# Kernel tuning notes

Measured on AMD Instinct MI355X. Metric: run time of the kernel, lower is better.

Reference implementation:

```python
import jax, jax.numpy as jnp
import numpy as np

B, S, H, NH = 2, 2048, 1024, 16
HD = H // NH  # head_size = 64


def setup_inputs() -> dict:
    key = jax.random.key(0)
    ks = jax.random.split(key, 9)
    sc = 0.02
    return {
        "hidden_states": jax.random.normal(ks[0], (B, S, H), dtype=jnp.float32),
        "Wq": jax.random.normal(ks[1], (H, H), dtype=jnp.float32) * sc,
        "bq": jax.random.normal(ks[2], (H,), dtype=jnp.float32) * sc,
        "Wk": jax.random.normal(ks[3], (H, H), dtype=jnp.float32) * sc,
        "bk": jax.random.normal(ks[4], (H,), dtype=jnp.float32) * sc,
        "Wv": jax.random.normal(ks[5], (H, H), dtype=jnp.float32) * sc,
        "bv": jax.random.normal(ks[6], (H,), dtype=jnp.float32) * sc,
        "Wo": jax.random.normal(ks[7], (H, H), dtype=jnp.float32) * sc,
        "bo": jax.random.normal(ks[8], (H,), dtype=jnp.float32) * sc,
    }


def reference(hidden_states, Wq, bq, Wk, bk, Wv, bv, Wo, bo):
    b, s, h = hidden_states.shape
    # nn.Linear: y = x @ W.T + b
    q = hidden_states @ Wq.T + bq
    k = hidden_states @ Wk.T + bk
    v = hidden_states @ Wv.T + bv
    q = q.reshape(b, s, NH, HD)
    k = k.reshape(b, s, NH, HD)
    v = v.reshape(b, s, NH, HD)
    # scores: [b, heads, q, k]
    scores = jnp.einsum("bqhd,bkhd->bhqk", q, k) / jnp.sqrt(jnp.float32(HD))
    # causal mask: triu(ones, diagonal=1) positions set to -inf
    causal = jnp.triu(jnp.ones((s, s), dtype=bool), k=1)
    scores = jnp.where(causal[None, None], -jnp.inf, scores)
    attn = jax.nn.softmax(scores, axis=-1)
    ctx = jnp.einsum("bhqk,bkhd->bqhd", attn, v).reshape(b, s, h)
    return ctx @ Wo.T + bo
```

## Files before the change

kernel.cpp:

```cpp
#include <hip/hip_runtime.h>
#include <hip/hip_bf16.h>

#define B_  2
#define S_  2048
#define H_  1024
#define NH_ 16
#define HD_ 64

typedef unsigned short u16;
typedef unsigned int   u32;
typedef __attribute__((ext_vector_type(4))) float  f32x4;
typedef __attribute__((ext_vector_type(8))) __bf16 bf16x8;
typedef __attribute__((ext_vector_type(2))) unsigned int u32x2;
typedef __attribute__((ext_vector_type(4))) unsigned short u16x4;

__device__ __forceinline__ u16 f2bf(float f) {
  unsigned u = __builtin_bit_cast(unsigned, f);
  u += 0x7fffu + ((u >> 16) & 1u);
  return (u16)(u >> 16);
}
__device__ __forceinline__ u32 cvtpk(float lo, float hi) {
  u32 r;
  asm("v_cvt_pk_bf16_f32 %0, %1, %2" : "=v"(r) : "v"(lo), "v"(hi));
  return r;
}
__device__ __forceinline__ float ex2(float x) {
  float r;
  asm("v_exp_f32 %0, %1" : "=v"(r) : "v"(x));
  return r;
}

__device__ __forceinline__ void gload_lds16(const void* g, void* l) {
  __builtin_amdgcn_global_load_lds(
      (const __attribute__((address_space(1))) void*)g,
      (__attribute__((address_space(3))) void*)l, 16, 0, 0);
}

#define NX_ (4u * 1024u * 1024u)
__global__ __launch_bounds__(256) void cvt_all(const float* __restrict__ x,
                                               const float* __restrict__ w0, const float* __restrict__ w1,
                                               const float* __restrict__ w2, const float* __restrict__ w3,
                                               u16* __restrict__ xb,
                                               u16* __restrict__ o0, u16* __restrict__ o1,
                                               u16* __restrict__ o2, u16* __restrict__ o3) {
  size_t i4 = ((size_t)blockIdx.x * 256 + threadIdx.x) * 4;
  const float* src; u16* dst; size_t off;
  if (i4 < (size_t)NX_) { src = x; dst = xb; off = i4; }
  else {
    size_t j = i4 - NX_;
    int seg = (int)(j >> 20);
    off = j & ((1u << 20) - 1);
    src = seg == 0 ? w0 : seg == 1 ? w1 : seg == 2 ? w2 : w3;
    dst = seg == 0 ? o0 : seg == 1 ? o1 : seg == 2 ? o2 : o3;
  }
  float4 v = *reinterpret_cast<const float4*>(src + off);
  u16x4 o;
  o[0] = f2bf(v.x); o[1] = f2bf(v.y); o[2] = f2bf(v.z); o[3] = f2bf(v.w);
  *reinterpret_cast<u16x4*>(dst + off) = o;
}

__device__ __forceinline__ void store_out(float* C, size_t idx, float v) { C[idx] = v; }
__device__ __forceinline__ void store_out(u16* C, size_t idx, float v) { C[idx] = f2bf(v); }

template <int MI, typename OutT>
__device__ __forceinline__ void gemm_core(const u16* __restrict__ A, const u16* __restrict__ Bw,
                                          const float* __restrict__ bias, OutT* __restrict__ C,
                                          int M, int N, int K, float oscale, int m0, int n0,
                                          u16* lsA, u16* lsB) {
  const int t = threadIdx.x;
  const int w = t >> 6, lane = t & 63;
  const int g = lane >> 4, c = lane & 15;
  const int wr = w >> 1, wc = w & 1;

  f32x4 acc[MI][4] = {};
  const int rowS = w * 16 + (lane >> 2);
  const int colS = (lane & 3) * 8;

  for (int k0 = 0; k0 < K; k0 += 32) {
    __syncthreads();
#pragma unroll
    for (int r = 0; r < MI / 2; ++r)
      gload_lds16(A + (size_t)(m0 + r * 64 + rowS) * K + k0 + colS, lsA + r * 2048 + w * 512);
#pragma unroll
    for (int r = 0; r < 2; ++r)
      gload_lds16(Bw + (size_t)(n0 + r * 64 + rowS) * K + k0 + colS, lsB + r * 2048 + w * 512);
    asm volatile("s_waitcnt vmcnt(0)" ::: "memory");
    __syncthreads();

    bf16x8 af[MI], bfr[4];
#pragma unroll
    for (int mi = 0; mi < MI; ++mi)
      af[mi] = *reinterpret_cast<const bf16x8*>(&lsA[(wr * (MI * 16) + mi * 16 + c) * 32 + g * 8]);
#pragma unroll
    for (int ni = 0; ni < 4; ++ni)
      bfr[ni] = *reinterpret_cast<const bf16x8*>(&lsB[(wc * 64 + ni * 16 + c) * 32 + g * 8]);
#pragma unroll
    for (int mi = 0; mi < MI; ++mi)
#pragma unroll
      for (int ni = 0; ni < 4; ++ni)
        acc[mi][ni] = __builtin_amdgcn_mfma_f32_16x16x32_bf16(af[mi], bfr[ni], acc[mi][ni], 0, 0, 0);
  }

#pragma unroll
  for (int mi = 0; mi < MI; ++mi) {
    int rowb = m0 + wr * (MI * 16) + mi * 16 + g * 4;
#pragma unroll
    for (int ni = 0; ni < 4; ++ni) {
      int col = n0 + wc * 64 + ni * 16 + c;
      float bv = bias[col];
#pragma unroll
      for (int r = 0; r < 4; ++r) {
        float v = (acc[mi][ni][r] + bv) * oscale;
        store_out(C, (size_t)(rowb + r) * N + col, v);
      }
    }
  }
}

__global__ __launch_bounds__(256) void gemm_qkv(const u16* __restrict__ xb,
                                                const u16* __restrict__ Wq, const u16* __restrict__ Wk,
                                                const u16* __restrict__ Wv,
                                                const float* __restrict__ bq, const float* __restrict__ bk,
                                                const float* __restrict__ bv,
                                                u16* __restrict__ Q, u16* __restrict__ Kb, u16* __restrict__ Vb,
                                                int M, int K, float qscale) {
  __shared__ u16 lsA[4096];
  __shared__ u16 lsB[4096];
  const int fid = blockIdx.x;
  const int xcd = fid & 7, i = fid >> 3;
  const int mloc = i / 24, nn = i % 24;
  const int m0 = (xcd * 4 + mloc) * 128;
  const int ng = nn * 128;
  const int sel = ng >> 10, n0 = ng & 1023;
  const u16*  W    = sel == 0 ? Wq : sel == 1 ? Wk : Wv;
  const float* bia = sel == 0 ? bq : sel == 1 ? bk : bv;
  u16*        Cp   = sel == 0 ? Q  : sel == 1 ? Kb : Vb;
  float os = sel == 0 ? qscale : 1.0f;
  gemm_core<4, u16>(xb, W, bia, Cp, M, 1024, K, os, m0, n0, lsA, lsB);
}

__global__ __launch_bounds__(256) void gemm_wo(const u16* __restrict__ A, const u16* __restrict__ Bw,
                                               const float* __restrict__ bias, float* __restrict__ C,
                                               int M, int N, int K) {
  __shared__ u16 lsA[2048];
  __shared__ u16 lsB[4096];
  const int fid = blockIdx.x;
  const int xcd = fid & 7, i = fid >> 3;
  const int mloc = i >> 3, nn = i & 7;
  const int m0 = (xcd * 8 + mloc) * 64;
  const int n0 = nn * 128;
  gemm_core<2, float>(A, Bw, bias, C, M, N, K, 1.0f, m0, n0, lsA, lsB);
}

__device__ __forceinline__ void stage_k(const u16* __restrict__ Kg, size_t headoff, int kvb,
                                        int kRow0, int kColB, int w, u16* lsKbuf) {
#pragma unroll
  for (int r = 0; r < 2; ++r)
    gload_lds16((const char*)(Kg + headoff + (size_t)(kvb + r * 32 + kRow0) * H_) + kColB,
                (char*)lsKbuf + r * 4096 + w * 1024);
}

__global__ __launch_bounds__(256) void attn_fwd(const u16* __restrict__ Qg,
                                                const u16* __restrict__ Kg,
                                                const u16* __restrict__ Vg,
                                                u16* __restrict__ Og) {
  __shared__ u16 lsK[2][64 * 64];
  __shared__ u16 lsVt[2][64 * 72];
  __shared__ u16 lsP[4][16 * 72];

  const int blk = blockIdx.x;
  const int xcd = blk & 7, i = blk >> 3;
  const int pair = i & 3;
  const int qt = 31 - (i >> 2);
  const int bh = xcd * 4 + pair;
  const int h = bh & 15, b = bh >> 4;

  const int t = threadIdx.x, w = t >> 6, lane = t & 63;
  const int g = lane >> 4, c = lane & 15;
  const size_t headoff = (size_t)b * (S_ * H_) + (size_t)h * HD_;
  const int q0 = qt * 64 + w * 16;
  const int nt = qt + 1;

  const int kO    = w * 1024 + lane * 16;
  const int kRow0 = kO >> 7;
  const int kColB = (kO & 127) ^ ((kRow0 & 7) << 4);
  const int vKv = 2 * (t >> 4);
  const int vD0 = 4 * (t & 15);
  const int vS  = 8 * ((vD0 >> 3) & 7);

  int qkOff[4][2], pvOff[4][2];
#pragma unroll
  for (int nj = 0; nj < 4; ++nj) {
    int krow = nj * 16 + c, sw = (krow & 7) << 4;
    qkOff[nj][0] = krow * 128 + ((g * 16) ^ sw);
    qkOff[nj][1] = krow * 128 + ((64 + g * 16) ^ sw);
  }
#pragma unroll
  for (int dt = 0; dt < 4; ++dt) {
    int d = dt * 16 + c, sx = ((d >> 3) & 7) << 4;
    pvOff[dt][0] = d * 144 + ((g * 16) ^ sx);
    pvOff[dt][1] = d * 144 + ((64 + g * 16) ^ sx);
  }

  bf16x8 aq0 = *reinterpret_cast<const bf16x8*>(Qg + headoff + (size_t)(q0 + c) * H_ + g * 8);
  bf16x8 aq1 = *reinterpret_cast<const bf16x8*>(Qg + headoff + (size_t)(q0 + c) * H_ + 32 + g * 8);

  f32x4 oacc[4] = {};
  float mrun = -1e30f, lrun = 0.f;
  u32x2 vlo[2], vhi[2];

#pragma unroll
  for (int r = 0; r < 2; ++r) {
    const u16* vp = Vg + headoff + (size_t)(r * 32 + vKv) * H_ + vD0;
    vlo[r] = *reinterpret_cast<const u32x2*>(vp);
    vhi[r] = *reinterpret_cast<const u32x2*>(vp + H_);
  }
  stage_k(Kg, headoff, 0, kRow0, kColB, w, lsK[0]);
  asm volatile("s_waitcnt vmcnt(2)" ::: "memory");
#pragma unroll
  for (int r = 0; r < 2; ++r) {
    int kvx = (r * 32 + vKv) ^ vS;
    u32 w0 = __builtin_amdgcn_perm(vhi[r][0], vlo[r][0], 0x05040100u);
    u32 w1 = __builtin_amdgcn_perm(vhi[r][0], vlo[r][0], 0x07060302u);
    u32 w2 = __builtin_amdgcn_perm(vhi[r][1], vlo[r][1], 0x05040100u);
    u32 w3 = __builtin_amdgcn_perm(vhi[r][1], vlo[r][1], 0x07060302u);
    *reinterpret_cast<u32*>(&lsVt[0][(vD0 + 0) * 72 + kvx]) = w0;
    *reinterpret_cast<u32*>(&lsVt[0][(vD0 + 1) * 72 + kvx]) = w1;
    *reinterpret_cast<u32*>(&lsVt[0][(vD0 + 2) * 72 + kvx]) = w2;
    *reinterpret_cast<u32*>(&lsVt[0][(vD0 + 3) * 72 + kvx]) = w3;
  }
  __syncthreads();

  for (int kt = 0; kt < nt; ++kt) {
    const int cur = kt & 1;
    const int kv0 = kt * 64;
    const bool st = (kt + 1 < nt);
    if (st) {
#pragma unroll
      for (int r = 0; r < 2; ++r) {
        const u16* vp = Vg + headoff + (size_t)(kv0 + 64 + r * 32 + vKv) * H_ + vD0;
        vlo[r] = *reinterpret_cast<const u32x2*>(vp);
        vhi[r] = *reinterpret_cast<const u32x2*>(vp + H_);
      }
      stage_k(Kg, headoff, kv0 + 64, kRow0, kColB, w, lsK[cur ^ 1]);
    }

    const char* kb = (const char*)lsK[cur];
    f32x4 sc[4];
#pragma unroll
    for (int nj = 0; nj < 4; ++nj) {
      bf16x8 ak0 = *reinterpret_cast<const bf16x8*>(kb + qkOff[nj][0]);
      bf16x8 ak1 = *reinterpret_cast<const bf16x8*>(kb + qkOff[nj][1]);
      f32x4 z = {};
      z = __builtin_amdgcn_mfma_f32_16x16x32_bf16(ak0, aq0, z, 0, 0, 0);
      z = __builtin_amdgcn_mfma_f32_16x16x32_bf16(ak1, aq1, z, 0, 0, 0);
      sc[nj] = z;
    }

    if (kt == qt) {
#pragma unroll
      for (int nj = 0; nj < 4; ++nj)
#pragma unroll
        for (int r = 0; r < 4; ++r) {
          int kv = kv0 + nj * 16 + 4 * g + r;
          sc[nj][r] = (kv > q0 + c) ? -1e30f : sc[nj][r];
        }
    }

    float m01 = fmaxf(fmaxf(sc[0][0], sc[0][1]), fmaxf(sc[0][2], sc[0][3]));
    float m23 = fmaxf(fmaxf(sc[1][0], sc[1][1]), fmaxf(sc[1][2], sc[1][3]));
    float m45 = fmaxf(fmaxf(sc[2][0], sc[2][1]), fmaxf(sc[2][2], sc[2][3]));
    float m67 = fmaxf(fmaxf(sc[3][0], sc[3][1]), fmaxf(sc[3][2], sc[3][3]));
    float pm = fmaxf(fmaxf(m01, m23), fmaxf(m45, m67));
    pm = fmaxf(pm, __shfl_xor(pm, 16));
    pm = fmaxf(pm, __shfl_xor(pm, 32));

    if (!__all(pm <= mrun + 8.0f)) {
      float mn = fmaxf(mrun, pm);
      float s8 = ex2(mrun - mn);
      mrun = mn;
      lrun *= s8;
#pragma unroll
      for (int r = 0; r < 4; ++r) {
        float sr = __shfl(s8, 4 * g + r);
#pragma unroll
        for (int dt = 0; dt < 4; ++dt) oacc[dt][r] *= sr;
      }
    }

    if (st) {
      asm volatile("s_waitcnt vmcnt(2)" ::: "memory");
#pragma unroll
      for (int r = 0; r < 2; ++r) {
        int kvx = (r * 32 + vKv) ^ vS;
        u32 w0 = __builtin_amdgcn_perm(vhi[r][0], vlo[r][0], 0x05040100u);
        u32 w1 = __builtin_amdgcn_perm(vhi[r][0], vlo[r][0], 0x07060302u);
        u32 w2 = __builtin_amdgcn_perm(vhi[r][1], vlo[r][1], 0x05040100u);
        u32 w3 = __builtin_amdgcn_perm(vhi[r][1], vlo[r][1], 0x07060302u);
        u16* vt = &lsVt[cur ^ 1][0];
        *reinterpret_cast<u32*>(&vt[(vD0 + 0) * 72 + kvx]) = w0;
        *reinterpret_cast<u32*>(&vt[(vD0 + 1) * 72 + kvx]) = w1;
        *reinterpret_cast<u32*>(&vt[(vD0 + 2) * 72 + kvx]) = w2;
        *reinterpret_cast<u32*>(&vt[(vD0 + 3) * 72 + kvx]) = w3;
      }
    }

    float rsn[4];
    u32x2 pp[4];
#pragma unroll
    for (int nj = 0; nj < 4; ++nj) {
      float p0 = ex2(sc[nj][0] - mrun);
      float p1 = ex2(sc[nj][1] - mrun);
      float p2 = ex2(sc[nj][2] - mrun);
      float p3 = ex2(sc[nj][3] - mrun);
      rsn[nj] = (p0 + p1) + (p2 + p3);
      pp[nj][0] = cvtpk(p0, p1);
      pp[nj][1] = cvtpk(p2, p3);
    }
    float rs = (rsn[0] + rsn[1]) + (rsn[2] + rsn[3]);
    rs += __shfl_xor(rs, 16);
    rs += __shfl_xor(rs, 32);
    lrun += rs;

#pragma unroll
    for (int nj = 0; nj < 4; ++nj)
      *reinterpret_cast<u32x2*>(&lsP[w][c * 72 + 16 * nj + 4 * g]) = pp[nj];
    asm volatile("s_waitcnt lgkmcnt(0)" ::: "memory");
    __builtin_amdgcn_sched_barrier(0);
    bf16x8 pa0 = *reinterpret_cast<const bf16x8*>(&lsP[w][c * 72 + g * 8]);
    bf16x8 pa1 = *reinterpret_cast<const bf16x8*>(&lsP[w][c * 72 + 32 + g * 8]);

    const char* vb = (const char*)lsVt[cur];
#pragma unroll
    for (int dt = 0; dt < 4; ++dt) {
      bf16x8 bv0 = *reinterpret_cast<const bf16x8*>(vb + pvOff[dt][0]);
      bf16x8 bv1 = *reinterpret_cast<const bf16x8*>(vb + pvOff[dt][1]);
      oacc[dt] = __builtin_amdgcn_mfma_f32_16x16x32_bf16(pa0, bv0, oacc[dt], 0, 0, 0);
      oacc[dt] = __builtin_amdgcn_mfma_f32_16x16x32_bf16(pa1, bv1, oacc[dt], 0, 0, 0);
    }

    __syncthreads();
  }

#pragma unroll
  for (int r = 0; r < 4; ++r) {
    float lq  = __shfl(lrun, 4 * g + r);
    float inv = 1.f / lq;
    int qrow  = q0 + 4 * g + r;
#pragma unroll
    for (int dt = 0; dt < 4; ++dt)
      Og[headoff + (size_t)qrow * H_ + dt * 16 + c] = f2bf(oacc[dt][r] * inv);
  }
}

extern "C" void kernel_launch(void* const* d_in, const int* in_sizes, int n_in,
                              void* d_out, int out_size, void* d_ws, size_t ws_size,
                              hipStream_t stream) {
  const float* x  = (const float*)d_in[0];
  const float* Wq = (const float*)d_in[1];
  const float* bq = (const float*)d_in[2];
  const float* Wk = (const float*)d_in[3];
  const float* bk = (const float*)d_in[4];
  const float* Wv = (const float*)d_in[5];
  const float* bv = (const float*)d_in[6];
  const float* Wo = (const float*)d_in[7];
  const float* bo = (const float*)d_in[8];
  float* out = (float*)d_out;

  const size_t MT = (size_t)B_ * S_;
  char* p = (char*)d_ws;
  u16* xb  = (u16*)p; p += MT * H_ * 2;
  u16* Wqb = (u16*)p; p += (size_t)H_ * H_ * 2;
  u16* Wkb = (u16*)p; p += (size_t)H_ * H_ * 2;
  u16* Wvb = (u16*)p; p += (size_t)H_ * H_ * 2;
  u16* Wob = (u16*)p; p += (size_t)H_ * H_ * 2;
  u16* Qb  = (u16*)p; p += MT * H_ * 2;
  u16* Kb  = (u16*)p; p += MT * H_ * 2;
  u16* Vb  = (u16*)p; p += MT * H_ * 2;
  u16* Cb  = xb;

  cvt_all<<<8192, 256, 0, stream>>>(x, Wq, Wk, Wv, Wo, xb, Wqb, Wkb, Wvb, Wob);

  const float qscale = 0.125f * 1.44269504088896f;
  gemm_qkv<<<768, 256, 0, stream>>>(xb, Wqb, Wkb, Wvb, bq, bk, bv,
                                    Qb, Kb, Vb, (int)MT, H_, qscale);

  attn_fwd<<<1024, 256, 0, stream>>>(Qb, Kb, Vb, Cb);

  gemm_wo<<<512, 256, 0, stream>>>(Cb, Wob, bo, out, (int)MT, H_, H_);
}
```

Before: 115.6 us.

## Restructure attention kernel with 32x32 MFMA and split-KV waves merged at end

Rewrites the attention kernel so that each pair of waves covers a 32-query slice using 32x32x16 MFMAs, and the two wave pairs take alternating 64-key tiles (split-KV inside the block). The partial softmax states are merged through shared memory at the end. P is passed to the PV MFMA through cross-lane shuffles instead of an LDS round trip, the causal diagonal tile skips its fully masked half, and the output is written with 16-byte stores. The aim is fewer LDS trips and better MFMA efficiency. In exchange the double-buffered prefetch is dropped in favour of a load/vmcnt(0)/sync step per pair of tiles, which adds load latency, and a combine phase is added at the end.

```diff
diff --git a/kernel.cpp b/kernel.cpp
--- a/kernel.cpp
+++ b/kernel.cpp
@@ -9,10 +9,12 @@
 
 typedef unsigned short u16;
 typedef unsigned int   u32;
-typedef __attribute__((ext_vector_type(4))) float  f32x4;
-typedef __attribute__((ext_vector_type(8))) __bf16 bf16x8;
-typedef __attribute__((ext_vector_type(2))) unsigned int u32x2;
-typedef __attribute__((ext_vector_type(4))) unsigned short u16x4;
+typedef __attribute__((ext_vector_type(4)))  float  f32x4;
+typedef __attribute__((ext_vector_type(16))) float  f32x16;
+typedef __attribute__((ext_vector_type(8)))  __bf16 bf16x8;
+typedef __attribute__((ext_vector_type(2)))  unsigned int u32x2;
+typedef __attribute__((ext_vector_type(4)))  unsigned int u32x4;
+typedef __attribute__((ext_vector_type(4)))  unsigned short u16x4;
 
 __device__ __forceinline__ u16 f2bf(float f) {
   unsigned u = __builtin_bit_cast(unsigned, f);
@@ -160,26 +162,83 @@
                 (char*)lsKbuf + r * 4096 + w * 1024);
 }
 
-__global__ __launch_bounds__(256) void attn_fwd(const u16* __restrict__ Qg,
-                                                const u16* __restrict__ Kg,
-                                                const u16* __restrict__ Vg,
-                                                u16* __restrict__ Og) {
-  __shared__ u16 lsK[2][64 * 64];
-  __shared__ u16 lsVt[2][64 * 72];
-  __shared__ u16 lsP[4][16 * 72];
+__device__ __forceinline__ void write_vt(u16* dst, const u32x2* va, const u32x2* vb,
+                                         int vKv, int vD0, int vS) {
+#pragma unroll
+  for (int r = 0; r < 2; ++r) {
+    int kvx = (r * 32 + vKv) ^ vS;
+    u32 w0 = __builtin_amdgcn_perm(vb[r][0], va[r][0], 0x05040100u);
+    u32 w1 = __builtin_amdgcn_perm(vb[r][0], va[r][0], 0x07060302u);
+    u32 w2 = __builtin_amdgcn_perm(vb[r][1], va[r][1], 0x05040100u);
+    u32 w3 = __builtin_amdgcn_perm(vb[r][1], va[r][1], 0x07060302u);
+    *reinterpret_cast<u32*>(dst + (vD0 + 0) * 72 + kvx) = w0;
+    *reinterpret_cast<u32*>(dst + (vD0 + 1) * 72 + kvx) = w1;
+    *reinterpret_cast<u32*>(dst + (vD0 + 2) * 72 + kvx) = w2;
+    *reinterpret_cast<u32*>(dst + (vD0 + 3) * 72 + kvx) = w3;
+  }
+}
+
+__device__ __forceinline__ void pv_sub(const f32x16& sc, float mrun, int ktbase,
+                                       const char* vtb, int hi, int c5,
+                                       f32x16& o0, f32x16& o1, float& rs) {
+  float p[16];
+#pragma unroll
+  for (int r = 0; r < 16; ++r) p[r] = ex2(sc[r] - mrun);
+  rs += ((p[0] + p[1]) + (p[2] + p[3])) + ((p[4] + p[5]) + (p[6] + p[7]))
+      + ((p[8] + p[9]) + (p[10] + p[11])) + ((p[12] + p[13]) + (p[14] + p[15]));
+  u32 wd[4][2];
+#pragma unroll
+  for (int a = 0; a < 4; ++a) {
+    wd[a][0] = cvtpk(p[4 * a + 0], p[4 * a + 1]);
+    wd[a][1] = cvtpk(p[4 * a + 2], p[4 * a + 3]);
+  }
+#pragma unroll
+  for (int ktp = 0; ktp < 2; ++ktp) {
+    u32 mw[4];
+#pragma unroll
+    for (int u = 0; u < 2; ++u) {
+      u32 A  = wd[2 * ktp][u], Bv = wd[2 * ktp + 1][u];
+      u32 oA = (u32)__shfl_xor((int)A, 32);
+      u32 oB = (u32)__shfl_xor((int)Bv, 32);
+      mw[u]     = hi ? oB : A;
+      mw[2 + u] = hi ? Bv : oA;
+    }
+    u32x4 pw = {mw[0], mw[1], mw[2], mw[3]};
+    bf16x8 pb = __builtin_bit_cast(bf16x8, pw);
+    const int kt = ktbase + ktp;
+#pragma unroll
+    for (int dt = 0; dt < 2; ++dt) {
+      int d = 32 * dt + c5;
+      int col = (kt * 32 + hi * 16) ^ (16 * ((d >> 3) & 7));
+      bf16x8 av = *reinterpret_cast<const bf16x8*>(vtb + d * 144 + col);
+      f32x16& oo = dt ? o1 : o0;
+      oo = __builtin_amdgcn_mfma_f32_32x32x16_bf16(av, pb, oo, 0, 0, 0);
+    }
+  }
+}
+
+__global__ __launch_bounds__(256, 4) void attn_fwd(const u16* __restrict__ Qg,
+                                                   const u16* __restrict__ Kg,
+                                                   const u16* __restrict__ Vg,
+                                                   u16* __restrict__ Og) {
+  __shared__ __align__(16) char smem[34816];
+  u16* lsK  = (u16*)smem;
+  u16* lsVt = (u16*)(smem + 16384);
+  float* lsO  = (float*)smem;
+  float* lsML = (float*)(smem + 20480);
+  u16*   lsOT = (u16*)(smem + 21504);
 
   const int blk = blockIdx.x;
   const int xcd = blk & 7, i = blk >> 3;
-  const int pair = i & 3;
-  const int qt = 31 - (i >> 2);
-  const int bh = xcd * 4 + pair;
+  const int qt  = 31 - (i >> 2);
+  const int bh  = xcd * 4 + (i & 3);
   const int h = bh & 15, b = bh >> 4;
 
   const int t = threadIdx.x, w = t >> 6, lane = t & 63;
-  const int g = lane >> 4, c = lane & 15;
+  const int sub = w & 1, par = w >> 1;
+  const int c5 = lane & 31, hi = lane >> 5;
   const size_t headoff = (size_t)b * (S_ * H_) + (size_t)h * HD_;
-  const int q0 = qt * 64 + w * 16;
-  const int nt = qt + 1;
+  const int q0w = qt * 64 + 32 * sub;
 
   const int kO    = w * 1024 + lane * 16;
   const int kRow0 = kO >> 7;
@@ -188,168 +247,150 @@
   const int vD0 = 4 * (t & 15);
   const int vS  = 8 * ((vD0 >> 3) & 7);
 
-  int qkOff[4][2], pvOff[4][2];
-#pragma unroll
-  for (int nj = 0; nj < 4; ++nj) {
-    int krow = nj * 16 + c, sw = (krow & 7) << 4;
-    qkOff[nj][0] = krow * 128 + ((g * 16) ^ sw);
-    qkOff[nj][1] = krow * 128 + ((64 + g * 16) ^ sw);
-  }
-#pragma unroll
-  for (int dt = 0; dt < 4; ++dt) {
-    int d = dt * 16 + c, sx = ((d >> 3) & 7) << 4;
-    pvOff[dt][0] = d * 144 + ((g * 16) ^ sx);
-    pvOff[dt][1] = d * 144 + ((64 + g * 16) ^ sx);
-  }
-
-  bf16x8 aq0 = *reinterpret_cast<const bf16x8*>(Qg + headoff + (size_t)(q0 + c) * H_ + g * 8);
-  bf16x8 aq1 = *reinterpret_cast<const bf16x8*>(Qg + headoff + (size_t)(q0 + c) * H_ + 32 + g * 8);
-
-  f32x4 oacc[4] = {};
+  bf16x8 aq[4];
+#pragma unroll
+  for (int kt = 0; kt < 4; ++kt)
+    aq[kt] = *reinterpret_cast<const bf16x8*>(Qg + headoff + (size_t)(q0w + c5) * H_ + kt * 16 + hi * 8);
+
+  f32x16 oacc0 = {}, oacc1 = {};
   float mrun = -1e30f, lrun = 0.f;
-  u32x2 vlo[2], vhi[2];
-
-#pragma unroll
-  for (int r = 0; r < 2; ++r) {
-    const u16* vp = Vg + headoff + (size_t)(r * 32 + vKv) * H_ + vD0;
-    vlo[r] = *reinterpret_cast<const u32x2*>(vp);
-    vhi[r] = *reinterpret_cast<const u32x2*>(vp + H_);
-  }
-  stage_k(Kg, headoff, 0, kRow0, kColB, w, lsK[0]);
-  asm volatile("s_waitcnt vmcnt(2)" ::: "memory");
-#pragma unroll
-  for (int r = 0; r < 2; ++r) {
-    int kvx = (r * 32 + vKv) ^ vS;
-    u32 w0 = __builtin_amdgcn_perm(vhi[r][0], vlo[r][0], 0x05040100u);
-    u32 w1 = __builtin_amdgcn_perm(vhi[r][0], vlo[r][0], 0x07060302u);
-    u32 w2 = __builtin_amdgcn_perm(vhi[r][1], vlo[r][1], 0x05040100u);
-    u32 w3 = __builtin_amdgcn_perm(vhi[r][1], vlo[r][1], 0x07060302u);
-    *reinterpret_cast<u32*>(&lsVt[0][(vD0 + 0) * 72 + kvx]) = w0;
-    *reinterpret_cast<u32*>(&lsVt[0][(vD0 + 1) * 72 + kvx]) = w1;
-    *reinterpret_cast<u32*>(&lsVt[0][(vD0 + 2) * 72 + kvx]) = w2;
-    *reinterpret_cast<u32*>(&lsVt[0][(vD0 + 3) * 72 + kvx]) = w3;
+
+  const int NIT = (qt >> 1) + 1;
+  for (int n = 0; n < NIT; ++n) {
+    const int kvb0 = 2 * n * 64;
+    const bool has1 = (2 * n + 1) <= qt;
+
+    u32x2 va0[2], vb0[2], va1[2], vb1[2];
+#pragma unroll
+    for (int r = 0; r < 2; ++r) {
+      const u16* vp = Vg + headoff + (size_t)(kvb0 + r * 32 + vKv) * H_ + vD0;
+      va0[r] = *reinterpret_cast<const u32x2*>(vp);
+      vb0[r] = *reinterpret_cast<const u32x2*>(vp + H_);
+    }
+    if (has1) {
+#pragma unroll
+      for (int r = 0; r < 2; ++r) {
+        const u16* vp = Vg + headoff + (size_t)(kvb0 + 64 + r * 32 + vKv) * H_ + vD0;
+        va1[r] = *reinterpret_cast<const u32x2*>(vp);
+        vb1[r] = *reinterpret_cast<const u32x2*>(vp + H_);
+      }
+    }
+    stage_k(Kg, headoff, kvb0, kRow0, kColB, w, lsK);
+    if (has1) stage_k(Kg, headoff, kvb0 + 64, kRow0, kColB, w, lsK + 4096);
+    asm volatile("s_waitcnt vmcnt(0)" ::: "memory");
+    write_vt(lsVt, va0, vb0, vKv, vD0, vS);
+    if (has1) write_vt(lsVt + 4608, va1, vb1, vKv, vD0, vS);
+    __syncthreads();
+
+    const int myt = 2 * n + par;
+    if (myt <= qt) {
+      const char* kb  = (const char*)lsK  + par * 8192;
+      const char* vtb = (const char*)lsVt + par * 9216;
+      const int nkv = (myt == qt && sub == 0) ? 1 : 2;
+
+      f32x16 sc0 = {}, sc1 = {};
+      __builtin_amdgcn_s_setprio(1);
+#pragma unroll
+      for (int kt = 0; kt < 4; ++kt) {
+        int colx = (kt * 32 + hi * 16) ^ ((c5 & 7) << 4);
+        bf16x8 ak0 = *reinterpret_cast<const bf16x8*>(kb + c5 * 128 + colx);
+        sc0 = __builtin_amdgcn_mfma_f32_32x32x16_bf16(ak0, aq[kt], sc0, 0, 0, 0);
+      }
+      if (nkv == 2) {
+#pragma unroll
+        for (int kt = 0; kt < 4; ++kt) {
+          int colx = (kt * 32 + hi * 16) ^ ((c5 & 7) << 4);
+          bf16x8 ak1 = *reinterpret_cast<const bf16x8*>(kb + (32 + c5) * 128 + colx);
+          sc1 = __builtin_amdgcn_mfma_f32_32x32x16_bf16(ak1, aq[kt], sc1, 0, 0, 0);
+        }
+      }
+      __builtin_amdgcn_s_setprio(0);
+
+      if (myt == qt) {
+        const int qg = q0w + c5;
+#pragma unroll
+        for (int r = 0; r < 16; ++r) {
+          int kvg = myt * 64 + (r & 3) + 8 * (r >> 2) + 4 * hi;
+          sc0[r] = (kvg > qg) ? -1e30f : sc0[r];
+          if (nkv == 2) sc1[r] = (kvg + 32 > qg) ? -1e30f : sc1[r];
+        }
+      }
+
+      float pm = sc0[0];
+#pragma unroll
+      for (int r = 1; r < 16; ++r) pm = fmaxf(pm, sc0[r]);
+      if (nkv == 2) {
+#pragma unroll
+        for (int r = 0; r < 16; ++r) pm = fmaxf(pm, sc1[r]);
+      }
+      pm = fmaxf(pm, (float)__shfl_xor(pm, 32));
+
+      if (!__all(pm <= mrun + 8.0f)) {
+        float mn = fmaxf(mrun, pm);
+        float s8 = ex2(mrun - mn);
+        mrun = mn; lrun *= s8;
+#pragma unroll
+        for (int r = 0; r < 16; ++r) { oacc0[r] *= s8; oacc1[r] *= s8; }
+      }
+
+      float rs = 0.f;
+      pv_sub(sc0, mrun, 0, vtb, hi, c5, oacc0, oacc1, rs);
+      if (nkv == 2) pv_sub(sc1, mrun, 2, vtb, hi, c5, oacc0, oacc1, rs);
+      rs += (float)__shfl_xor(rs, 32);
+      lrun += rs;
+    }
+    __syncthreads();
+  }
+
+  if (par == 0) {
+    if (hi == 0) { lsML[sub * 64 + c5] = mrun; lsML[sub * 64 + 32 + c5] = lrun; }
+#pragma unroll
+    for (int dt = 0; dt < 2; ++dt) {
+      float* dst = lsO + ((size_t)((sub * 2 + dt) * 64 + lane)) * 20;
+      const f32x16& oo = dt ? oacc1 : oacc0;
+#pragma unroll
+      for (int k4 = 0; k4 < 4; ++k4) {
+        f32x4 v4 = {oo[4 * k4], oo[4 * k4 + 1], oo[4 * k4 + 2], oo[4 * k4 + 3]};
+        *reinterpret_cast<f32x4*>(dst + 4 * k4) = v4;
+      }
+    }
   }
   __syncthreads();
-
-  for (int kt = 0; kt < nt; ++kt) {
-    const int cur = kt & 1;
-    const int kv0 = kt * 64;
-    const bool st = (kt + 1 < nt);
-    if (st) {
-#pragma unroll
-      for (int r = 0; r < 2; ++r) {
-        const u16* vp = Vg + headoff + (size_t)(kv0 + 64 + r * 32 + vKv) * H_ + vD0;
-        vlo[r] = *reinterpret_cast<const u32x2*>(vp);
-        vhi[r] = *reinterpret_cast<const u32x2*>(vp + H_);
-      }
-      stage_k(Kg, headoff, kv0 + 64, kRow0, kColB, w, lsK[cur ^ 1]);
-    }
-
-    const char* kb = (const char*)lsK[cur];
-    f32x4 sc[4];
-#pragma unroll
-    for (int nj = 0; nj < 4; ++nj) {
-      bf16x8 ak0 = *reinterpret_cast<const bf16x8*>(kb + qkOff[nj][0]);
-      bf16x8 ak1 = *reinterpret_cast<const bf16x8*>(kb + qkOff[nj][1]);
-      f32x4 z = {};
-      z = __builtin_amdgcn_mfma_f32_16x16x32_bf16(ak0, aq0, z, 0, 0, 0);
-      z = __builtin_amdgcn_mfma_f32_16x16x32_bf16(ak1, aq1, z, 0, 0, 0);
-      sc[nj] = z;
-    }
-
-    if (kt == qt) {
-#pragma unroll
-      for (int nj = 0; nj < 4; ++nj)
-#pragma unroll
-        for (int r = 0; r < 4; ++r) {
-          int kv = kv0 + nj * 16 + 4 * g + r;
-          sc[nj][r] = (kv > q0 + c) ? -1e30f : sc[nj][r];
+  if (par == 1) {
+    float mA = lsML[sub * 64 + c5];
+    float lA = lsML[sub * 64 + 32 + c5];
+    float mn = fmaxf(mA, mrun);
+    float sA = ex2(mA - mn), sB = ex2(mrun - mn);
+    float linv = 1.0f / (lA * sA + lrun * sB);
+    sA *= linv; sB *= linv;
+    u16* ot = lsOT + sub * 32 * 72;
+#pragma unroll
+    for (int dt = 0; dt < 2; ++dt) {
+      const float* sp = lsO + ((size_t)((sub * 2 + dt) * 64 + lane)) * 20;
+      f32x4 a4[4];
+#pragma unroll
+      for (int k4 = 0; k4 < 4; ++k4) a4[k4] = *reinterpret_cast<const f32x4*>(sp + 4 * k4);
+      const f32x16& oo = dt ? oacc1 : oacc0;
+#pragma unroll
+      for (int a = 0; a < 4; ++a)
+#pragma unroll
+        for (int u = 0; u < 2; ++u) {
+          int r = 4 * a + 2 * u;
+          float o0 = a4[a][2 * u]     * sA + oo[r]     * sB;
+          float o1 = a4[a][2 * u + 1] * sA + oo[r + 1] * sB;
+          int d = 32 * dt + 8 * a + 4 * hi + 2 * u;
+          *reinterpret_cast<u32*>(ot + c5 * 72 + d) = cvtpk(o0, o1);
         }
     }
-
-    float m01 = fmaxf(fmaxf(sc[0][0], sc[0][1]), fmaxf(sc[0][2], sc[0][3]));
-    float m23 = fmaxf(fmaxf(sc[1][0], sc[1][1]), fmaxf(sc[1][2], sc[1][3]));
-    float m45 = fmaxf(fmaxf(sc[2][0], sc[2][1]), fmaxf(sc[2][2], sc[2][3]));
-    float m67 = fmaxf(fmaxf(sc[3][0], sc[3][1]), fmaxf(sc[3][2], sc[3][3]));
-    float pm = fmaxf(fmaxf(m01, m23), fmaxf(m45, m67));
-    pm = fmaxf(pm, __shfl_xor(pm, 16));
-    pm = fmaxf(pm, __shfl_xor(pm, 32));
-
-    if (!__all(pm <= mrun + 8.0f)) {
-      float mn = fmaxf(mrun, pm);
-      float s8 = ex2(mrun - mn);
-      mrun = mn;
-      lrun *= s8;
-#pragma unroll
-      for (int r = 0; r < 4; ++r) {
-        float sr = __shfl(s8, 4 * g + r);
-#pragma unroll
-        for (int dt = 0; dt < 4; ++dt) oacc[dt][r] *= sr;
-      }
-    }
-
-    if (st) {
-      asm volatile("s_waitcnt vmcnt(2)" ::: "memory");
-#pragma unroll
-      for (int r = 0; r < 2; ++r) {
-        int kvx = (r * 32 + vKv) ^ vS;
-        u32 w0 = __builtin_amdgcn_perm(vhi[r][0], vlo[r][0], 0x05040100u);
-        u32 w1 = __builtin_amdgcn_perm(vhi[r][0], vlo[r][0], 0x07060302u);
-        u32 w2 = __builtin_amdgcn_perm(vhi[r][1], vlo[r][1], 0x05040100u);
-        u32 w3 = __builtin_amdgcn_perm(vhi[r][1], vlo[r][1], 0x07060302u);
-        u16* vt = &lsVt[cur ^ 1][0];
-        *reinterpret_cast<u32*>(&vt[(vD0 + 0) * 72 + kvx]) = w0;
-        *reinterpret_cast<u32*>(&vt[(vD0 + 1) * 72 + kvx]) = w1;
-        *reinterpret_cast<u32*>(&vt[(vD0 + 2) * 72 + kvx]) = w2;
-        *reinterpret_cast<u32*>(&vt[(vD0 + 3) * 72 + kvx]) = w3;
-      }
-    }
-
-    float rsn[4];
-    u32x2 pp[4];
-#pragma unroll
-    for (int nj = 0; nj < 4; ++nj) {
-      float p0 = ex2(sc[nj][0] - mrun);
-      float p1 = ex2(sc[nj][1] - mrun);
-      float p2 = ex2(sc[nj][2] - mrun);
-      float p3 = ex2(sc[nj][3] - mrun);
-      rsn[nj] = (p0 + p1) + (p2 + p3);
-      pp[nj][0] = cvtpk(p0, p1);
-      pp[nj][1] = cvtpk(p2, p3);
-    }
-    float rs = (rsn[0] + rsn[1]) + (rsn[2] + rsn[3]);
-    rs += __shfl_xor(rs, 16);
-    rs += __shfl_xor(rs, 32);
-    lrun += rs;
-
-#pragma unroll
-    for (int nj = 0; nj < 4; ++nj)
-      *reinterpret_cast<u32x2*>(&lsP[w][c * 72 + 16 * nj + 4 * g]) = pp[nj];
     asm volatile("s_waitcnt lgkmcnt(0)" ::: "memory");
     __builtin_amdgcn_sched_barrier(0);
-    bf16x8 pa0 = *reinterpret_cast<const bf16x8*>(&lsP[w][c * 72 + g * 8]);
-    bf16x8 pa1 = *reinterpret_cast<const bf16x8*>(&lsP[w][c * 72 + 32 + g * 8]);
-
-    const char* vb = (const char*)lsVt[cur];
-#pragma unroll
-    for (int dt = 0; dt < 4; ++dt) {
-      bf16x8 bv0 = *reinterpret_cast<const bf16x8*>(vb + pvOff[dt][0]);
-      bf16x8 bv1 = *reinterpret_cast<const bf16x8*>(vb + pvOff[dt][1]);
-      oacc[dt] = __builtin_amdgcn_mfma_f32_16x16x32_bf16(pa0, bv0, oacc[dt], 0, 0, 0);
-      oacc[dt] = __builtin_amdgcn_mfma_f32_16x16x32_bf16(pa1, bv1, oacc[dt], 0, 0, 0);
-    }
-
-    __syncthreads();
-  }
-
-#pragma unroll
-  for (int r = 0; r < 4; ++r) {
-    float lq  = __shfl(lrun, 4 * g + r);
-    float inv = 1.f / lq;
-    int qrow  = q0 + 4 * g + r;
-#pragma unroll
-    for (int dt = 0; dt < 4; ++dt)
-      Og[headoff + (size_t)qrow * H_ + dt * 16 + c] = f2bf(oacc[dt][r] * inv);
+#pragma unroll
+    for (int rr = 0; rr < 4; ++rr) {
+      int q = 8 * rr + (lane >> 3);
+      int d8 = (lane & 7) * 8;
+      u32x4 vv = *reinterpret_cast<const u32x4*>(ot + q * 72 + d8);
+      *reinterpret_cast<u32x4*>(Og + headoff + (size_t)(qt * 64 + 32 * sub + q) * H_ + d8) = vv;
+    }
   }
 }
 
```

Result: faster. 113.2 us (-2.1%).
